# Performance work log

Hardware: AMD Instinct MI355X
Metric: run time of the kernel (lower is better)

Reference implementation:

```python
import jax, jax.numpy as jnp
import numpy as np

BZ, SRC_LEN, TGT_LEN, DIM = 32, 1024, 1024, 512


def setup_inputs() -> dict:
    key = jax.random.key(0)
    k1, k2, k3, k4 = jax.random.split(key, 4)
    src = jax.random.normal(k1, (BZ, SRC_LEN, DIM), dtype=jnp.float32)
    tgt = jax.random.normal(k2, (BZ, TGT_LEN, DIM), dtype=jnp.float32)
    # lengths in [1, SRC_LEN] so every row has at least one valid position
    src_lengths = jax.random.randint(k3, (BZ,), 1, SRC_LEN + 1, dtype=jnp.int64)
    # nn.Linear(2*dim, dim, bias=False): weight shape (dim, 2*dim)
    bound = 1.0 / np.sqrt(2 * DIM)
    w_out = jax.random.uniform(k4, (DIM, 2 * DIM), dtype=jnp.float32,
                               minval=-bound, maxval=bound)
    return {"src": src, "tgt": tgt, "src_lengths": src_lengths, "w_out": w_out}


def reference(src, tgt, src_lengths, w_out):
    # dot-product attention scores: (bz, tgt_len, src_len)
    score = jnp.einsum("btd,bsd->bts", tgt, src)
    # mask out padded source positions (position >= length)
    valid = jnp.arange(src.shape[1])[None, :] < src_lengths[:, None]  # (bz, src_len)
    score = jnp.where(valid[:, None, :], score, -jnp.inf)
    align = jax.nn.softmax(score, axis=-1)
    # context: (bz, tgt_len, dim)
    c = jnp.einsum("bts,bsd->btd", align, src)
    concat_c = jnp.concatenate([c, tgt], axis=-1)  # (bz, tgt_len, 2*dim)
    attn_h = jnp.einsum("bte,de->btd", concat_c, w_out)
    return attn_h, align
```

## Files before the change

### kernel.cpp

```cpp
#include <hip/hip_runtime.h>
#include <hip/hip_bf16.h>

typedef __attribute__((ext_vector_type(4))) float  f32x4;
typedef __attribute__((ext_vector_type(4))) float  float4v;
typedef __attribute__((ext_vector_type(8))) short  bf16x8;
typedef __attribute__((ext_vector_type(4))) short  bf16x4;
typedef __attribute__((ext_vector_type(2))) unsigned int u32x2;

#define BZ   32
#define SLEN 1024
#define TLEN 1024
#define DIM  512
#define TILE 128
#define LP   40

#define PSEL 0x07060302u

__device__ __forceinline__ unsigned int fbits(float x) { return __builtin_bit_cast(unsigned int, x); }
__device__ __forceinline__ float fval(unsigned int u) { return __builtin_bit_cast(float, u); }

__device__ __forceinline__ unsigned short f2bf(float x) {
  unsigned int u = fbits(x);
  unsigned int r = u + 0x7FFFu + ((u >> 16) & 1u);
  return (unsigned short)(r >> 16);
}
__device__ __forceinline__ float bf2f(unsigned short h) { return fval(((unsigned int)h) << 16); }

__device__ __forceinline__ unsigned int packhi(float x0, float x1) {
  return __builtin_amdgcn_perm(fbits(x1), fbits(x0), PSEL);
}

__device__ __forceinline__ int get_len(const int* __restrict__ p, int b) {
  bool is64 = (p[1] == 0) && (p[3] == 0) && (p[5] == 0);
  return is64 ? p[2 * b] : p[b];
}

#define TLP 68
__global__ __launch_bounds__(256) void k_transpose(
    const float* __restrict__ src, unsigned short* __restrict__ srcT) {
  const int b  = blockIdx.z;
  const int s0 = blockIdx.x * 64;
  const int d0 = blockIdx.y * 64;
  __shared__ unsigned short tl[64 * TLP];
  const int tid = threadIdx.x;
#pragma unroll
  for (int r = 0; r < 4; ++r) {
    const int idx = tid + 256 * r;
    const int row = idx >> 4, c4 = idx & 15;
    float4v x = *(const float4v*)(src + ((size_t)(b * SLEN + s0 + row)) * DIM + d0 + c4 * 4);
    unsigned short* pp = tl + row * TLP + c4 * 4;
    pp[0] = f2bf(x[0]); pp[1] = f2bf(x[1]); pp[2] = f2bf(x[2]); pp[3] = f2bf(x[3]);
  }
  __syncthreads();
#pragma unroll
  for (int r = 0; r < 2; ++r) {
    const int idx  = tid + 256 * r;
    const int drow = idx >> 3, c8 = idx & 7;
    union { unsigned short u[8]; bf16x8 v; } pk;
#pragma unroll
    for (int j = 0; j < 8; ++j) pk.u[j] = tl[(c8 * 8 + j) * TLP + drow];
    *(bf16x8*)(srcT + ((size_t)(b * DIM + d0 + drow)) * SLEN + s0 + c8 * 8) = pk.v;
  }
}

__global__ __launch_bounds__(256) void k_prep_w(
    const float* __restrict__ w, unsigned short* __restrict__ wbf) {
  const size_t i = ((size_t)blockIdx.x * 256 + threadIdx.x) * 8;
  float4v x0 = *(const float4v*)(w + i);
  float4v x1 = *(const float4v*)(w + i + 4);
  union { unsigned short u[8]; bf16x8 v; } hi;
#pragma unroll
  for (int j = 0; j < 4; ++j) { hi.u[j] = f2bf(x0[j]); hi.u[4 + j] = f2bf(x1[j]); }
  *(bf16x8*)(wbf + i) = hi.v;
}

__global__ __launch_bounds__(256) void k_score(
    const float* __restrict__ tgt, const float* __restrict__ src,
    const int* __restrict__ lens, float* __restrict__ align_out) {
  const int b  = blockIdx.z;
  const int t0 = blockIdx.x * TILE;
  const int s0 = blockIdx.y * TILE;
  const int len = get_len(lens, b);
  if (s0 >= len) return;

  __shared__ short aHi[TILE * LP], aLo[TILE * LP], bHi[TILE * LP], bLo[TILE * LP];

  const int tid  = threadIdx.x;
  const int lane = tid & 63;
  const int wid  = tid >> 6;
  const int wt   = wid >> 1, wsd = wid & 1;
  const int g    = lane >> 4, r16 = lane & 15;
  const int srow = tid >> 3, sc4 = tid & 7;

  f32x4 acc[4][4];
#pragma unroll
  for (int m = 0; m < 4; ++m)
#pragma unroll
    for (int n = 0; n < 4; ++n) acc[m][n] = (f32x4){0.f, 0.f, 0.f, 0.f};

  const float* tgtB = tgt + ((size_t)(b * TLEN + t0)) * DIM;
  const float* srcB = src + ((size_t)(b * SLEN + s0)) * DIM;

  float4v va[4], vb[4];
#pragma unroll
  for (int r = 0; r < 4; ++r) {
    const int row = srow + 32 * r;
    va[r] = *(const float4v*)(tgtB + (size_t)row * DIM + sc4 * 4);
    vb[r] = *(const float4v*)(srcB + (size_t)row * DIM + sc4 * 4);
  }

  for (int k0 = 0; k0 < DIM; k0 += 32) {
#pragma unroll
    for (int r = 0; r < 4; ++r) {
      const int row = srow + 32 * r;
      u32x2 ah, al, bh, bl;
      ah[0] = packhi(va[r][0], va[r][1]); ah[1] = packhi(va[r][2], va[r][3]);
      bh[0] = packhi(vb[r][0], vb[r][1]); bh[1] = packhi(vb[r][2], vb[r][3]);
      float ra0 = va[r][0] - fval(fbits(va[r][0]) & 0xFFFF0000u);
      float ra1 = va[r][1] - fval(fbits(va[r][1]) & 0xFFFF0000u);
      float ra2 = va[r][2] - fval(fbits(va[r][2]) & 0xFFFF0000u);
      float ra3 = va[r][3] - fval(fbits(va[r][3]) & 0xFFFF0000u);
      float rb0 = vb[r][0] - fval(fbits(vb[r][0]) & 0xFFFF0000u);
      float rb1 = vb[r][1] - fval(fbits(vb[r][1]) & 0xFFFF0000u);
      float rb2 = vb[r][2] - fval(fbits(vb[r][2]) & 0xFFFF0000u);
      float rb3 = vb[r][3] - fval(fbits(vb[r][3]) & 0xFFFF0000u);
      al[0] = packhi(ra0, ra1); al[1] = packhi(ra2, ra3);
      bl[0] = packhi(rb0, rb1); bl[1] = packhi(rb2, rb3);
      const int o = row * LP + sc4 * 4;
      *(u32x2*)(aHi + o) = ah; *(u32x2*)(aLo + o) = al;
      *(u32x2*)(bHi + o) = bh; *(u32x2*)(bLo + o) = bl;
    }
    if (k0 + 32 < DIM) {
#pragma unroll
      for (int r = 0; r < 4; ++r) {
        const int row = srow + 32 * r;
        va[r] = *(const float4v*)(tgtB + (size_t)row * DIM + (k0 + 32) + sc4 * 4);
        vb[r] = *(const float4v*)(srcB + (size_t)row * DIM + (k0 + 32) + sc4 * 4);
      }
    }
    __syncthreads();
    bf16x8 fbh[4], fbl[4];
#pragma unroll
    for (int n = 0; n < 4; ++n) {
      const int row = wsd * 64 + n * 16 + r16;
      fbh[n] = *(const bf16x8*)(bHi + row * LP + g * 8);
      fbl[n] = *(const bf16x8*)(bLo + row * LP + g * 8);
    }
#pragma unroll
    for (int m = 0; m < 4; ++m) {
      const int row = wt * 64 + m * 16 + r16;
      bf16x8 fah = *(const bf16x8*)(aHi + row * LP + g * 8);
      bf16x8 fal = *(const bf16x8*)(aLo + row * LP + g * 8);
#pragma unroll
      for (int n = 0; n < 4; ++n) {
        acc[m][n] = __builtin_amdgcn_mfma_f32_16x16x32_bf16(fah, fbh[n], acc[m][n], 0, 0, 0);
        acc[m][n] = __builtin_amdgcn_mfma_f32_16x16x32_bf16(fal, fbh[n], acc[m][n], 0, 0, 0);
        acc[m][n] = __builtin_amdgcn_mfma_f32_16x16x32_bf16(fah, fbl[n], acc[m][n], 0, 0, 0);
      }
    }
    __syncthreads();
  }
  float* outB = align_out + ((size_t)(b * TLEN + t0)) * SLEN + s0;
#pragma unroll
  for (int m = 0; m < 4; ++m) {
    const int tr = wt * 64 + m * 16 + g * 4;
#pragma unroll
    for (int n = 0; n < 4; ++n) {
      const int sc = wsd * 64 + n * 16 + r16;
#pragma unroll
      for (int r = 0; r < 4; ++r)
        outB[(size_t)(tr + r) * SLEN + sc] = acc[m][n][r];
    }
  }
}

__global__ __launch_bounds__(256) void k_softmax(
    const int* __restrict__ lens, float* __restrict__ align_io) {
  const int row  = blockIdx.x * 4 + (threadIdx.x >> 6);
  const int lane = threadIdx.x & 63;
  const int b    = row >> 10;
  const int len  = get_len(lens, b);
  float* p = align_io + (size_t)row * SLEN;
  float v[4][4];
  float mx = -3.0e38f;
#pragma unroll
  for (int q = 0; q < 4; ++q) {
    const int sb = (lane + 64 * q) * 4;
    float4v x = *(const float4v*)(p + sb);
#pragma unroll
    for (int j = 0; j < 4; ++j) {
      v[q][j] = x[j];
      if (sb + j < len) mx = fmaxf(mx, x[j]);
    }
  }
#pragma unroll
  for (int off = 1; off < 64; off <<= 1) mx = fmaxf(mx, __shfl_xor(mx, off));
  float sum = 0.f;
#pragma unroll
  for (int q = 0; q < 4; ++q) {
    const int sb = (lane + 64 * q) * 4;
#pragma unroll
    for (int j = 0; j < 4; ++j) {
      float e = (sb + j < len) ? __expf(v[q][j] - mx) : 0.f;
      v[q][j] = e; sum += e;
    }
  }
#pragma unroll
  for (int off = 1; off < 64; off <<= 1) sum += __shfl_xor(sum, off);
  const float inv = 1.f / sum;
#pragma unroll
  for (int q = 0; q < 4; ++q) {
    float4v x;
#pragma unroll
    for (int j = 0; j < 4; ++j) x[j] = v[q][j] * inv;
    *(float4v*)(p + (lane + 64 * q) * 4) = x;
  }
}

__global__ __launch_bounds__(256) void k_pv(
    const float* __restrict__ align_in, const unsigned short* __restrict__ srcT,
    const int* __restrict__ lens, unsigned short* __restrict__ cws) {
  const int b  = blockIdx.z;
  const int t0 = blockIdx.x * TILE;
  const int d0 = blockIdx.y * TILE;
  const int len = get_len(lens, b);
  const int ksteps = (len + 31) >> 5;

  __shared__ short A[TILE * LP], B[TILE * LP];
  const int tid  = threadIdx.x;
  const int lane = tid & 63;
  const int wid  = tid >> 6;
  const int wt   = wid >> 1, wsd = wid & 1;
  const int g    = lane >> 4, r16 = lane & 15;

  f32x4 acc[4][4];
#pragma unroll
  for (int m = 0; m < 4; ++m)
#pragma unroll
    for (int n = 0; n < 4; ++n) acc[m][n] = (f32x4){0.f, 0.f, 0.f, 0.f};

  const int arow = tid >> 3, ac4 = tid & 7;
  const int brow = tid >> 2, bc8 = tid & 3;

  float4v xa[4];
  bf16x8  xb[2];
#pragma unroll
  for (int r = 0; r < 4; ++r)
    xa[r] = *(const float4v*)(align_in + ((size_t)(b * TLEN + t0 + arow + 32 * r)) * SLEN + ac4 * 4);
#pragma unroll
  for (int r = 0; r < 2; ++r)
    xb[r] = *(const bf16x8*)(srcT + ((size_t)(b * DIM + d0 + brow + 64 * r)) * SLEN + bc8 * 8);

  for (int ks = 0; ks < ksteps; ++ks) {
#pragma unroll
    for (int r = 0; r < 4; ++r) {
      u32x2 h;
      h[0] = packhi(xa[r][0], xa[r][1]); h[1] = packhi(xa[r][2], xa[r][3]);
      *(u32x2*)(A + (arow + 32 * r) * LP + ac4 * 4) = h;
    }
#pragma unroll
    for (int r = 0; r < 2; ++r)
      *(bf16x8*)(B + (brow + 64 * r) * LP + bc8 * 8) = xb[r];
    if (ks + 1 < ksteps) {
      const int k0 = (ks + 1) * 32;
#pragma unroll
      for (int r = 0; r < 4; ++r)
        xa[r] = *(const float4v*)(align_in + ((size_t)(b * TLEN + t0 + arow + 32 * r)) * SLEN + k0 + ac4 * 4);
#pragma unroll
      for (int r = 0; r < 2; ++r)
        xb[r] = *(const bf16x8*)(srcT + ((size_t)(b * DIM + d0 + brow + 64 * r)) * SLEN + k0 + bc8 * 8);
    }
    __syncthreads();
    bf16x8 fb[4];
#pragma unroll
    for (int n = 0; n < 4; ++n) fb[n] = *(const bf16x8*)(B + (wsd * 64 + n * 16 + r16) * LP + g * 8);
#pragma unroll
    for (int m = 0; m < 4; ++m) {
      bf16x8 fa = *(const bf16x8*)(A + (wt * 64 + m * 16 + r16) * LP + g * 8);
#pragma unroll
      for (int n = 0; n < 4; ++n)
        acc[m][n] = __builtin_amdgcn_mfma_f32_16x16x32_bf16(fa, fb[n], acc[m][n], 0, 0, 0);
    }
    __syncthreads();
  }
#pragma unroll
  for (int m = 0; m < 4; ++m) {
    const int tr = wt * 64 + m * 16 + g * 4;
#pragma unroll
    for (int n = 0; n < 4; ++n) {
      const int dc = wsd * 64 + n * 16 + r16;
#pragma unroll
      for (int r = 0; r < 4; ++r)
        cws[((size_t)(b * TLEN + t0 + tr + r)) * DIM + d0 + dc] = f2bf(acc[m][n][r]);
    }
  }
}

__global__ __launch_bounds__(256) void k_proj(
    const unsigned short* __restrict__ cws, const float* __restrict__ tgt,
    const unsigned short* __restrict__ wbf, float* __restrict__ attn_out) {
  const int b  = blockIdx.z;
  const int t0 = blockIdx.x * TILE;
  const int d0 = blockIdx.y * TILE;

  __shared__ short A[TILE * LP], B[TILE * LP];
  const int tid  = threadIdx.x;
  const int lane = tid & 63;
  const int wid  = tid >> 6;
  const int wt   = wid >> 1, wsd = wid & 1;
  const int g    = lane >> 4, r16 = lane & 15;

  f32x4 acc[4][4];
#pragma unroll
  for (int m = 0; m < 4; ++m)
#pragma unroll
    for (int n = 0; n < 4; ++n) acc[m][n] = (f32x4){0.f, 0.f, 0.f, 0.f};

  for (int k0 = 0; k0 < 2 * DIM; k0 += 32) {
    if (k0 < DIM) {
#pragma unroll
      for (int r = 0; r < 2; ++r) {
        const int row = (tid >> 2) + 64 * r, c8 = tid & 3;
        bf16x8 x = *(const bf16x8*)(cws + ((size_t)(b * TLEN + t0 + row)) * DIM + k0 + c8 * 8);
        *(bf16x8*)(A + row * LP + c8 * 8) = x;
      }
    } else {
#pragma unroll
      for (int r = 0; r < 4; ++r) {
        const int row = (tid >> 3) + 32 * r, c4 = tid & 7;
        float4v x = *(const float4v*)(tgt + ((size_t)(b * TLEN + t0 + row)) * DIM + (k0 - DIM) + c4 * 4);
        bf16x4 h;
#pragma unroll
        for (int j = 0; j < 4; ++j) h[j] = (short)f2bf(x[j]);
        *(bf16x4*)(A + row * LP + c4 * 4) = h;
      }
    }
#pragma unroll
    for (int r = 0; r < 2; ++r) {
      const int row = (tid >> 2) + 64 * r, c8 = tid & 3;
      bf16x8 x = *(const bf16x8*)(wbf + ((size_t)(d0 + row)) * (2 * DIM) + k0 + c8 * 8);
      *(bf16x8*)(B + row * LP + c8 * 8) = x;
    }
    __syncthreads();
    bf16x8 fb[4];
#pragma unroll
    for (int n = 0; n < 4; ++n) fb[n] = *(const bf16x8*)(B + (wsd * 64 + n * 16 + r16) * LP + g * 8);
#pragma unroll
    for (int m = 0; m < 4; ++m) {
      bf16x8 fa = *(const bf16x8*)(A + (wt * 64 + m * 16 + r16) * LP + g * 8);
#pragma unroll
      for (int n = 0; n < 4; ++n)
        acc[m][n] = __builtin_amdgcn_mfma_f32_16x16x32_bf16(fa, fb[n], acc[m][n], 0, 0, 0);
    }
    __syncthreads();
  }
#pragma unroll
  for (int m = 0; m < 4; ++m) {
    const int tr = wt * 64 + m * 16 + g * 4;
#pragma unroll
    for (int n = 0; n < 4; ++n) {
      const int dc = wsd * 64 + n * 16 + r16;
#pragma unroll
      for (int r = 0; r < 4; ++r)
        attn_out[((size_t)(b * TLEN + t0 + tr + r)) * DIM + d0 + dc] = acc[m][n][r];
    }
  }
}

extern "C" void kernel_launch(void* const* d_in, const int* in_sizes, int n_in,
                              void* d_out, int out_size, void* d_ws, size_t ws_size,
                              hipStream_t stream) {
  const float* src   = (const float*)d_in[0];
  const float* tgt   = (const float*)d_in[1];
  const int*   lens  = (const int*)d_in[2];
  const float* w_out = (const float*)d_in[3];

  float* attn_out  = (float*)d_out;
  float* align_out = attn_out + (size_t)BZ * TLEN * DIM;

  const size_t NE = (size_t)BZ * SLEN * DIM;
  const size_t NW = (size_t)DIM * 2 * DIM;
  unsigned short* srcT = (unsigned short*)d_ws;
  unsigned short* cws  = srcT + NE;
  unsigned short* wbf  = cws + NE;

  k_transpose<<<dim3(16, 8, BZ), 256, 0, stream>>>(src, srcT);
  k_prep_w<<<dim3((unsigned)(NW / 8 / 256)), 256, 0, stream>>>(w_out, wbf);
  k_score<<<dim3(8, 8, BZ), 256, 0, stream>>>(tgt, src, lens, align_out);
  k_softmax<<<dim3(BZ * TLEN / 4), 256, 0, stream>>>(lens, align_out);
  k_pv<<<dim3(8, 4, BZ), 256, 0, stream>>>(align_out, srcT, lens, cws);
  k_proj<<<dim3(8, 4, BZ), 256, 0, stream>>>(cws, tgt, wbf, attn_out);
}
```

Measured before the change: 263.0 us.

## Compact score tiles by batch length and schedule longest batches first

Adds a tiny kernel that sorts batches by source length and builds prefix offsets of the live score tiles. k_score then launches a flat 1D grid over only the live tiles, longest batches first, instead of a 3D grid where blocks past the length exit early. k_pv is reordered by the same length ranking, and softmax skips loading fully masked chunks. This aims to cut empty-block launch overhead and tail imbalance, at the cost of one extra launch and some index decoding per block.

```diff
diff --git a/kernel.cpp b/kernel.cpp
--- a/kernel.cpp
+++ b/kernel.cpp
@@ -33,6 +33,35 @@
 __device__ __forceinline__ int get_len(const int* __restrict__ p, int b) {
   bool is64 = (p[1] == 0) && (p[3] == 0) && (p[5] == 0);
   return is64 ? p[2 * b] : p[b];
+}
+
+__global__ __launch_bounds__(64) void k_count(
+    const int* __restrict__ lens, int* __restrict__ meta) {
+  __shared__ int sLen[32], sOrder[32], sNt[33];
+  const int lane = threadIdx.x;
+  if (lane < 32) sLen[lane] = get_len(lens, lane);
+  __syncthreads();
+  if (lane < 32) {
+    const int li = sLen[lane];
+    int rank = 0;
+#pragma unroll
+    for (int j = 0; j < 32; ++j) {
+      const int lj = sLen[j];
+      if (lj > li || (lj == li && j < lane)) ++rank;
+    }
+    sOrder[rank] = lane;
+  }
+  __syncthreads();
+  if (lane < 32) {
+    meta[lane] = sOrder[lane];
+    sNt[lane] = ((sLen[sOrder[lane]] + 127) >> 7) * 8;
+  }
+  __syncthreads();
+  if (lane == 0) {
+    int acc = 0;
+    meta[32] = 0;
+    for (int r = 0; r < 32; ++r) { acc += sNt[r]; meta[33 + r] = acc; }
+  }
 }
 
 #define TLP 68
@@ -76,16 +105,27 @@
 
 __global__ __launch_bounds__(256) void k_score(
     const float* __restrict__ tgt, const float* __restrict__ src,
-    const int* __restrict__ lens, float* __restrict__ align_out) {
-  const int b  = blockIdx.z;
-  const int t0 = blockIdx.x * TILE;
-  const int s0 = blockIdx.y * TILE;
-  const int len = get_len(lens, b);
-  if (s0 >= len) return;
-
+    const int* __restrict__ meta, float* __restrict__ align_out) {
   __shared__ short aHi[TILE * LP], aLo[TILE * LP], bHi[TILE * LP], bLo[TILE * LP];
+  __shared__ int sOrder[32], sOffs[33];
 
   const int tid  = threadIdx.x;
+  if (tid < 32) sOrder[tid] = meta[tid];
+  if (tid < 33) sOffs[tid] = meta[32 + tid];
+  __syncthreads();
+
+  const int item = blockIdx.x;
+  if (item >= sOffs[32]) return;
+
+  int r = 0;
+  while (sOffs[r + 1] <= item) ++r;
+  const int b      = sOrder[r];
+  const int within = item - sOffs[r];
+  const int nt     = (sOffs[r + 1] - sOffs[r]) >> 3;
+  const int t_idx  = within / nt;
+  const int s_idx  = within - t_idx * nt;
+  const int t0 = t_idx * TILE, s0 = s_idx * TILE;
+
   const int lane = tid & 63;
   const int wid  = tid >> 6;
   const int wt   = wid >> 1, wsd = wid & 1;
@@ -103,27 +143,27 @@
 
   float4v va[4], vb[4];
 #pragma unroll
-  for (int r = 0; r < 4; ++r) {
-    const int row = srow + 32 * r;
-    va[r] = *(const float4v*)(tgtB + (size_t)row * DIM + sc4 * 4);
-    vb[r] = *(const float4v*)(srcB + (size_t)row * DIM + sc4 * 4);
+  for (int r2 = 0; r2 < 4; ++r2) {
+    const int row = srow + 32 * r2;
+    va[r2] = *(const float4v*)(tgtB + (size_t)row * DIM + sc4 * 4);
+    vb[r2] = *(const float4v*)(srcB + (size_t)row * DIM + sc4 * 4);
   }
 
   for (int k0 = 0; k0 < DIM; k0 += 32) {
 #pragma unroll
-    for (int r = 0; r < 4; ++r) {
-      const int row = srow + 32 * r;
+    for (int r2 = 0; r2 < 4; ++r2) {
+      const int row = srow + 32 * r2;
       u32x2 ah, al, bh, bl;
-      ah[0] = packhi(va[r][0], va[r][1]); ah[1] = packhi(va[r][2], va[r][3]);
-      bh[0] = packhi(vb[r][0], vb[r][1]); bh[1] = packhi(vb[r][2], vb[r][3]);
-      float ra0 = va[r][0] - fval(fbits(va[r][0]) & 0xFFFF0000u);
-      float ra1 = va[r][1] - fval(fbits(va[r][1]) & 0xFFFF0000u);
-      float ra2 = va[r][2] - fval(fbits(va[r][2]) & 0xFFFF0000u);
-      float ra3 = va[r][3] - fval(fbits(va[r][3]) & 0xFFFF0000u);
-      float rb0 = vb[r][0] - fval(fbits(vb[r][0]) & 0xFFFF0000u);
-      float rb1 = vb[r][1] - fval(fbits(vb[r][1]) & 0xFFFF0000u);
-      float rb2 = vb[r][2] - fval(fbits(vb[r][2]) & 0xFFFF0000u);
-      float rb3 = vb[r][3] - fval(fbits(vb[r][3]) & 0xFFFF0000u);
+      ah[0] = packhi(va[r2][0], va[r2][1]); ah[1] = packhi(va[r2][2], va[r2][3]);
+      bh[0] = packhi(vb[r2][0], vb[r2][1]); bh[1] = packhi(vb[r2][2], vb[r2][3]);
+      float ra0 = va[r2][0] - fval(fbits(va[r2][0]) & 0xFFFF0000u);
+      float ra1 = va[r2][1] - fval(fbits(va[r2][1]) & 0xFFFF0000u);
+      float ra2 = va[r2][2] - fval(fbits(va[r2][2]) & 0xFFFF0000u);
+      float ra3 = va[r2][3] - fval(fbits(va[r2][3]) & 0xFFFF0000u);
+      float rb0 = vb[r2][0] - fval(fbits(vb[r2][0]) & 0xFFFF0000u);
+      float rb1 = vb[r2][1] - fval(fbits(vb[r2][1]) & 0xFFFF0000u);
+      float rb2 = vb[r2][2] - fval(fbits(vb[r2][2]) & 0xFFFF0000u);
+      float rb3 = vb[r2][3] - fval(fbits(vb[r2][3]) & 0xFFFF0000u);
       al[0] = packhi(ra0, ra1); al[1] = packhi(ra2, ra3);
       bl[0] = packhi(rb0, rb1); bl[1] = packhi(rb2, rb3);
       const int o = row * LP + sc4 * 4;
@@ -132,10 +172,10 @@
     }
     if (k0 + 32 < DIM) {
 #pragma unroll
-      for (int r = 0; r < 4; ++r) {
-        const int row = srow + 32 * r;
-        va[r] = *(const float4v*)(tgtB + (size_t)row * DIM + (k0 + 32) + sc4 * 4);
-        vb[r] = *(const float4v*)(srcB + (size_t)row * DIM + (k0 + 32) + sc4 * 4);
+      for (int r2 = 0; r2 < 4; ++r2) {
+        const int row = srow + 32 * r2;
+        va[r2] = *(const float4v*)(tgtB + (size_t)row * DIM + (k0 + 32) + sc4 * 4);
+        vb[r2] = *(const float4v*)(srcB + (size_t)row * DIM + (k0 + 32) + sc4 * 4);
       }
     }
     __syncthreads();
@@ -168,8 +208,8 @@
     for (int n = 0; n < 4; ++n) {
       const int sc = wsd * 64 + n * 16 + r16;
 #pragma unroll
-      for (int r = 0; r < 4; ++r)
-        outB[(size_t)(tr + r) * SLEN + sc] = acc[m][n][r];
+      for (int rr = 0; rr < 4; ++rr)
+        outB[(size_t)(tr + rr) * SLEN + sc] = acc[m][n][rr];
     }
   }
 }
@@ -185,11 +225,16 @@
   float mx = -3.0e38f;
 #pragma unroll
   for (int q = 0; q < 4; ++q) {
+    if (256 * q >= len) {
+#pragma unroll
+      for (int j = 0; j < 4; ++j) v[q][j] = 0.f;
+      continue;
+    }
     const int sb = (lane + 64 * q) * 4;
     float4v x = *(const float4v*)(p + sb);
 #pragma unroll
     for (int j = 0; j < 4; ++j) {
-      v[q][j] = x[j];
+      v[q][j] = (sb + j < len) ? x[j] : 0.f;
       if (sb + j < len) mx = fmaxf(mx, x[j]);
     }
   }
@@ -219,8 +264,9 @@
 
 __global__ __launch_bounds__(256) void k_pv(
     const float* __restrict__ align_in, const unsigned short* __restrict__ srcT,
-    const int* __restrict__ lens, unsigned short* __restrict__ cws) {
-  const int b  = blockIdx.z;
+    const int* __restrict__ lens, const int* __restrict__ meta,
+    unsigned short* __restrict__ cws) {
+  const int b  = meta[blockIdx.z];
   const int t0 = blockIdx.x * TILE;
   const int d0 = blockIdx.y * TILE;
   const int len = get_len(lens, b);
@@ -383,11 +429,13 @@
   unsigned short* srcT = (unsigned short*)d_ws;
   unsigned short* cws  = srcT + NE;
   unsigned short* wbf  = cws + NE;
-
+  int*            meta = (int*)(wbf + NW);
+
+  k_count<<<dim3(1), 64, 0, stream>>>(lens, meta);
   k_transpose<<<dim3(16, 8, BZ), 256, 0, stream>>>(src, srcT);
   k_prep_w<<<dim3((unsigned)(NW / 8 / 256)), 256, 0, stream>>>(w_out, wbf);
-  k_score<<<dim3(8, 8, BZ), 256, 0, stream>>>(tgt, src, lens, align_out);
+  k_score<<<dim3(2048), 256, 0, stream>>>(tgt, src, meta, align_out);
   k_softmax<<<dim3(BZ * TLEN / 4), 256, 0, stream>>>(lens, align_out);
-  k_pv<<<dim3(8, 4, BZ), 256, 0, stream>>>(align_out, srcT, lens, cws);
+  k_pv<<<dim3(8, 4, BZ), 256, 0, stream>>>(align_out, srcT, lens, meta, cws);
   k_proj<<<dim3(8, 4, BZ), 256, 0, stream>>>(cws, tgt, wbf, attn_out);
 }
```

Result: slower. 269.7 us (+2.5%).
